# Optimization experiments

Hardware: AMD Instinct MI355X
Metric: run time of the kernel (lower is better)

Reference implementation:

```python
import jax, jax.numpy as jnp
import numpy as np
import math

B, C, H, W = 16, 256, 48, 48
CK = C // 8


def setup_inputs() -> dict:
    key = jax.random.key(0)
    ks = jax.random.split(key, 8)
    s = 0.05
    return {
        "x": jax.random.normal(ks[0], (B, C, H, W), dtype=jnp.float32),
        "Wq": jax.random.normal(ks[1], (CK, C), dtype=jnp.float32) * s,
        "bq": jax.random.normal(ks[2], (CK,), dtype=jnp.float32) * s,
        "Wk": jax.random.normal(ks[3], (CK, C), dtype=jnp.float32) * s,
        "bk": jax.random.normal(ks[4], (CK,), dtype=jnp.float32) * s,
        "Wv": jax.random.normal(ks[5], (C, C), dtype=jnp.float32) * s,
        "bv": jax.random.normal(ks[6], (C,), dtype=jnp.float32) * s,
        "gamma": jax.random.normal(ks[7], (1,), dtype=jnp.float32) * 0.1,
    }


def reference(x, Wq, bq, Wk, bk, Wv, bv, gamma):
    b, c, h, w = x.shape
    n = h * w
    xf = x.reshape(b, c, n)  # [B, C, N] (1x1 conv == channel matmul)
    q = jnp.einsum("oc,bcn->bno", Wq, xf) + bq  # [B, N, C/8]
    k = jnp.einsum("oc,bcn->bon", Wk, xf) + bk[None, :, None]  # [B, C/8, N]
    v = jnp.einsum("oc,bcn->bon", Wv, xf) + bv[None, :, None]  # [B, C, N]
    # NOTE: original scales by sqrt(C) (d_k = C), not sqrt(C//8)
    energy = jnp.einsum("bnd,bdm->bnm", q, k) / math.sqrt(c)  # [B, N, N]
    attn = jax.nn.softmax(energy, axis=-1)
    # out[b,c,i] = sum_j v[b,c,j] * attn[b,i,j]
    out = jnp.einsum("bcj,bij->bci", v, attn).reshape(b, c, h, w)
    return gamma[0] * out + x
```

## Files before the change

### kernel.cpp

```cpp
#include <hip/hip_runtime.h>
#include <hip/hip_bf16.h>

#define Bn  16
#define Cn  256
#define CKn 32
#define Nn  2304

typedef __attribute__((ext_vector_type(16))) float f32x16;
typedef __attribute__((ext_vector_type(8)))  short bf16x8;
typedef __attribute__((ext_vector_type(4)))  int   i32x4;

union FragU { unsigned u[4]; bf16x8 v; };
union KU    { i32x4 i; bf16x8 v; };

__device__ __forceinline__ unsigned pk(float lo, float hi){
  unsigned a = (unsigned)__bfloat16_as_ushort(__float2bfloat16(lo));
  unsigned b = (unsigned)__bfloat16_as_ushort(__float2bfloat16(hi));
  return a | (b << 16);
}

__device__ __forceinline__ void halfswap(unsigned A, unsigned Bv, int ,
                                         unsigned &w0, unsigned &w2){
  asm("v_permlane32_swap_b32 %0, %1" : "+v"(A), "+v"(Bv));
  w0 = A; w2 = Bv;
}

__device__ __forceinline__ void conv_store(const f32x16& a, int h, int l,
                                           __hip_bfloat16* dst0, size_t stride){
  unsigned Wp[8];
  #pragma unroll
  for (int q = 0; q < 8; ++q) Wp[q] = pk(a[2*q], a[2*q+1]);
  #pragma unroll
  for (int k2 = 0; k2 < 2; ++k2){
    FragU u;
    halfswap(Wp[4*k2+0], Wp[4*k2+2], h, u.u[0], u.u[2]);
    halfswap(Wp[4*k2+1], Wp[4*k2+3], h, u.u[1], u.u[3]);
    *(bf16x8*)(dst0 + k2*stride + l*8) = u.v;
  }
}

__device__ __forceinline__ void gld16(const void* g, void* l){
  __builtin_amdgcn_global_load_lds(
      (__attribute__((address_space(1))) void*)const_cast<void*>(g),
      (__attribute__((address_space(3))) void*)l, 16, 0, 0);
}

__global__ __launch_bounds__(64) void wfrag_kernel(
    const float* __restrict__ Wq, const float* __restrict__ bq,
    const float* __restrict__ Wk, const float* __restrict__ bk,
    const float* __restrict__ Wv, const float* __restrict__ bv,
    __hip_bfloat16* __restrict__ Wf){
  const int kt = blockIdx.x / 10, tile = blockIdx.x % 10;
  const int l = threadIdx.x, lo = l & 31, h = l >> 5;
  __hip_bfloat16* dst = Wf + (size_t)(kt*10 + tile)*512 + l*8;
  if (kt < 16){
    const float* Wp; int row;
    if (tile < 8)       { Wp = Wv; row = tile*32 + lo; }
    else if (tile == 8) { Wp = Wq; row = lo; }
    else                { Wp = Wk; row = lo; }
    #pragma unroll
    for (int e = 0; e < 8; ++e)
      dst[e] = __float2bfloat16(Wp[(size_t)row*Cn + kt*16 + 8*h + e]);
  } else {
    const float* bp = tile < 8 ? bv : (tile == 8 ? bq : bk);
    int row = tile < 8 ? tile*32 + lo : lo;
    #pragma unroll
    for (int e = 0; e < 8; ++e)
      dst[e] = __float2bfloat16((h == 0 && e == 0) ? bp[row] : 0.f);
  }
}

__global__ __launch_bounds__(64) void proj_kernel(
    const float* __restrict__ x, const __hip_bfloat16* __restrict__ Wf,
    __hip_bfloat16* __restrict__ Qf, __hip_bfloat16* __restrict__ Kf,
    __hip_bfloat16* __restrict__ Vf){
  const int u = blockIdx.x;
  const int b = u / 72, n32 = u % 72;
  const int l = threadIdx.x & 63, lo = l & 31, h = l >> 5;
  const int n0 = n32*32;

  f32x16 acc[10];
  #pragma unroll
  for (int t = 0; t < 10; ++t)
    #pragma unroll
    for (int r = 0; r < 16; ++r) acc[t][r] = 0.f;

  const float* xb = x + (size_t)b*Cn*Nn + n0 + lo;

  #pragma unroll 1
  for (int kt = 0; kt < 16; ++kt){
    FragU xf;
    float v[8];
    #pragma unroll
    for (int e = 0; e < 8; ++e) v[e] = xb[(size_t)(kt*16 + 8*h + e)*Nn];
    #pragma unroll
    for (int q = 0; q < 4; ++q) xf.u[q] = pk(v[2*q], v[2*q+1]);
    const __hip_bfloat16* wfp = Wf + (size_t)(kt*10)*512 + l*8;
    #pragma unroll
    for (int t = 0; t < 10; ++t){
      bf16x8 wf = *(const bf16x8*)(wfp + t*512);
      if (t < 8) acc[t] = __builtin_amdgcn_mfma_f32_32x32x16_bf16(xf.v, wf, acc[t], 0,0,0);
      else       acc[t] = __builtin_amdgcn_mfma_f32_32x32x16_bf16(wf, xf.v, acc[t], 0,0,0);
    }
  }
  {
    FragU xf;
    xf.u[0] = h ? 0u : 0x00003f80u;
    xf.u[1] = xf.u[2] = xf.u[3] = 0u;
    const __hip_bfloat16* wfp = Wf + (size_t)(16*10)*512 + l*8;
    #pragma unroll
    for (int t = 0; t < 10; ++t){
      bf16x8 wf = *(const bf16x8*)(wfp + t*512);
      if (t < 8) acc[t] = __builtin_amdgcn_mfma_f32_32x32x16_bf16(xf.v, wf, acc[t], 0,0,0);
      else       acc[t] = __builtin_amdgcn_mfma_f32_32x32x16_bf16(wf, xf.v, acc[t], 0,0,0);
    }
  }

  #pragma unroll
  for (int r = 0; r < 16; ++r) acc[8][r] *= 0.09016844f;

  #pragma unroll
  for (int t = 0; t < 8; ++t)
    conv_store(acc[t], h, l, Vf + (((size_t)b*144 + n32*2)*8 + t)*512, 8*512);
  conv_store(acc[8], h, l, Qf + ((size_t)b*72 + n32)*2*512, 512);
  conv_store(acc[9], h, l, Kf + ((size_t)b*72 + n32)*2*512, 512);
}

__global__ __launch_bounds__(128, 2) void attn_kernel(
    const __hip_bfloat16* __restrict__ Qf, const __hip_bfloat16* __restrict__ Kf,
    const __hip_bfloat16* __restrict__ Vf, const float* __restrict__ x,
    const float* __restrict__ gptr, float* __restrict__ out){
  __shared__ __align__(16) char smem[32768];
  const int xcd = blockIdx.x & 7, seq = blockIdx.x >> 3;
  const int b    = xcd*2 + (seq / 72);
  const int rem  = seq % 72;
  const int qb   = rem >> 1;
  const int ch   = rem & 1;
  const int tid = threadIdx.x;
  const int w = tid >> 6, l = tid & 63, lo = l & 31, h = l >> 5;

  const char* vlane = (const char*)Vf + ((size_t)b*1152 + ch*4)*1024 + (size_t)l*16;
  const char* klane = (const char*)Kf + (size_t)b*147456 + (size_t)l*16;

  auto stageV = [&](int jt, int buf){
    const char* gt = vlane + (size_t)jt*32768;
    #pragma unroll
    for (int r = 0; r < 8; ++r){
      const int f = r*2 + w;
      gld16(gt + (f >> 2)*8192 + (f & 3)*1024, smem + buf*16384 + f*1024);
    }
  };
  auto kload = [&](int jn, KU (&kf)[2][2]){
    const char* ka = klane + (size_t)jn*4096;
    asm volatile("global_load_dwordx4 %0, %1, off"             : "=v"(kf[0][0].i) : "v"(ka) : "memory");
    asm volatile("global_load_dwordx4 %0, %1, off offset:1024" : "=v"(kf[0][1].i) : "v"(ka) : "memory");
    asm volatile("global_load_dwordx4 %0, %1, off offset:2048" : "=v"(kf[1][0].i) : "v"(ka) : "memory");
    asm volatile("global_load_dwordx4 %0, %1, off offset:3072" : "=v"(kf[1][1].i) : "v"(ka) : "memory");
  };

  bf16x8 qf[2];
  #pragma unroll
  for (int kt = 0; kt < 2; ++kt)
    qf[kt] = *(const bf16x8*)(Qf + (((size_t)b*72 + qb*2 + w)*2 + kt)*512 + l*8);

  f32x16 acc4[4];
  #pragma unroll
  for (int c = 0; c < 4; ++c)
    #pragma unroll
    for (int r = 0; r < 16; ++r) acc4[c][r] = 0.f;
  float lsum = 0.f;

  KU kfA[2][2], kfB[2][2];

  kload(0, kfA);
  stageV(0, 0);
  kload(1, kfB);

  auto body = [&](int jt, KU (&cur)[2][2], int vb){
    asm volatile("s_waitcnt vmcnt(4)" ::: "memory");
    __builtin_amdgcn_s_barrier();
    __builtin_amdgcn_sched_barrier(0);
    int jn = jt + 1; if (jn >= 36) jn -= 36;
    stageV(jn, vb ^ 1);

    f32x16 z;
    #pragma unroll
    for (int r = 0; r < 16; ++r) z[r] = 0.f;
    f32x16 S0 = __builtin_amdgcn_mfma_f32_32x32x16_bf16(cur[0][0].v, qf[0], z, 0,0,0);
    S0 = __builtin_amdgcn_mfma_f32_32x32x16_bf16(cur[0][1].v, qf[1], S0, 0,0,0);
    f32x16 S1 = __builtin_amdgcn_mfma_f32_32x32x16_bf16(cur[1][0].v, qf[0], z, 0,0,0);
    S1 = __builtin_amdgcn_mfma_f32_32x32x16_bf16(cur[1][1].v, qf[1], S1, 0,0,0);

    int j2 = jt + 2; if (j2 >= 36) j2 -= 36;
    kload(j2, cur);

    FragU pf[4];
    float s0 = 0.f, s1 = 0.f, s2 = 0.f, s3 = 0.f;
    {
      unsigned Wp[8];
      #pragma unroll
      for (int q = 0; q < 4; ++q){
        float p0 = __builtin_amdgcn_exp2f(S0[2*q]);
        float p1 = __builtin_amdgcn_exp2f(S0[2*q+1]);
        s0 += p0 + p1; Wp[q] = pk(p0, p1);
      }
      #pragma unroll
      for (int q = 4; q < 8; ++q){
        float p0 = __builtin_amdgcn_exp2f(S0[2*q]);
        float p1 = __builtin_amdgcn_exp2f(S0[2*q+1]);
        s1 += p0 + p1; Wp[q] = pk(p0, p1);
      }
      halfswap(Wp[0], Wp[2], h, pf[0].u[0], pf[0].u[2]);
      halfswap(Wp[1], Wp[3], h, pf[0].u[1], pf[0].u[3]);
      halfswap(Wp[4], Wp[6], h, pf[1].u[0], pf[1].u[2]);
      halfswap(Wp[5], Wp[7], h, pf[1].u[1], pf[1].u[3]);
    }
    {
      unsigned Wp[8];
      #pragma unroll
      for (int q = 0; q < 4; ++q){
        float p0 = __builtin_amdgcn_exp2f(S1[2*q]);
        float p1 = __builtin_amdgcn_exp2f(S1[2*q+1]);
        s2 += p0 + p1; Wp[q] = pk(p0, p1);
      }
      #pragma unroll
      for (int q = 4; q < 8; ++q){
        float p0 = __builtin_amdgcn_exp2f(S1[2*q]);
        float p1 = __builtin_amdgcn_exp2f(S1[2*q+1]);
        s3 += p0 + p1; Wp[q] = pk(p0, p1);
      }
      halfswap(Wp[0], Wp[2], h, pf[2].u[0], pf[2].u[2]);
      halfswap(Wp[1], Wp[3], h, pf[2].u[1], pf[2].u[3]);
      halfswap(Wp[4], Wp[6], h, pf[3].u[0], pf[3].u[2]);
      halfswap(Wp[5], Wp[7], h, pf[3].u[1], pf[3].u[3]);
    }
    lsum += (s0 + s1) + (s2 + s3);

    const char* cbV = smem + vb*16384;
    #pragma unroll
    for (int js = 0; js < 4; ++js){
      #pragma unroll
      for (int c = 0; c < 4; ++c){
        bf16x8 v = *(const bf16x8*)(cbV + (js*4 + c)*1024 + l*16);
        acc4[c] = __builtin_amdgcn_mfma_f32_32x32x16_bf16(v, pf[js].v, acc4[c], 0,0,0);
      }
    }
  };

  #pragma unroll 1
  for (int jt = 0; jt < 36; jt += 2){
    body(jt,   kfA, 0);
    body(jt+1, kfB, 1);
  }

  lsum += __shfl_xor(lsum, 32);
  const float sc = gptr[0] / lsum;
  const int ibase = qb*64 + w*32;
  #pragma unroll
  for (int c = 0; c < 4; ++c){
    #pragma unroll
    for (int r = 0; r < 16; ++r){
      const int cg = ch*128 + c*32 + (r & 3) + 8*(r >> 2) + 4*h;
      const size_t idx = ((size_t)b*Cn + cg)*Nn + ibase + lo;
      out[idx] = acc4[c][r]*sc + x[idx];
    }
  }
}

extern "C" void kernel_launch(void* const* d_in, const int* in_sizes, int n_in,
                              void* d_out, int out_size, void* d_ws, size_t ws_size,
                              hipStream_t stream) {
  const float* x     = (const float*)d_in[0];
  const float* Wq    = (const float*)d_in[1];
  const float* bq    = (const float*)d_in[2];
  const float* Wk    = (const float*)d_in[3];
  const float* bk    = (const float*)d_in[4];
  const float* Wv    = (const float*)d_in[5];
  const float* bv    = (const float*)d_in[6];
  const float* gamma = (const float*)d_in[7];
  float* out = (float*)d_out;

  __hip_bfloat16* Qf = (__hip_bfloat16*)d_ws;
  __hip_bfloat16* Kf = Qf + (size_t)Bn*72*2*512;
  __hip_bfloat16* Vf = Kf + (size_t)Bn*72*2*512;
  __hip_bfloat16* Wf = Vf + (size_t)Bn*144*8*512;

  wfrag_kernel<<<dim3(170), dim3(64), 0, stream>>>(Wq, bq, Wk, bk, Wv, bv, Wf);
  proj_kernel<<<dim3(1152), dim3(64), 0, stream>>>(x, Wf, Qf, Kf, Vf);
  attn_kernel<<<dim3(1152), dim3(128), 0, stream>>>(Qf, Kf, Vf, x, gamma, out);
}
```

Measured before the change: 107.2 us.

## Split attention blocks to single-wave with unshared single-buffered V staging

The attention kernel moves from 128-thread blocks (two waves sharing a double-buffered 32KB LDS V tile) to 64-thread single-wave blocks, each covering one 32-row query tile, launched as twice as many blocks. Each wave stages its own V tile into a single 16KB buffer and replaces the block barrier with vmcnt/lgkmcnt waits, prefetching K one step ahead instead of two. This removes cross-wave barriers and lets more blocks fit per CU. In exchange, V traffic from L2 per query row doubles, and single buffering exposes V load latency within each iteration.

```diff
diff --git a/kernel.cpp b/kernel.cpp
--- a/kernel.cpp
+++ b/kernel.cpp
@@ -126,29 +126,26 @@
   conv_store(acc[9], h, l, Kf + ((size_t)b*72 + n32)*2*512, 512);
 }
 
-__global__ __launch_bounds__(128, 2) void attn_kernel(
+__global__ __launch_bounds__(64, 2) void attn_kernel(
     const __hip_bfloat16* __restrict__ Qf, const __hip_bfloat16* __restrict__ Kf,
     const __hip_bfloat16* __restrict__ Vf, const float* __restrict__ x,
     const float* __restrict__ gptr, float* __restrict__ out){
-  __shared__ __align__(16) char smem[32768];
+  __shared__ __align__(16) char smem[16384];
   const int xcd = blockIdx.x & 7, seq = blockIdx.x >> 3;
-  const int b    = xcd*2 + (seq / 72);
-  const int rem  = seq % 72;
-  const int qb   = rem >> 1;
-  const int ch   = rem & 1;
-  const int tid = threadIdx.x;
-  const int w = tid >> 6, l = tid & 63, lo = l & 31, h = l >> 5;
+  const int b   = xcd*2 + (seq / 144);
+  const int rem = seq % 144;
+  const int qt  = rem >> 1;
+  const int ch  = rem & 1;
+  const int l = threadIdx.x & 63, lo = l & 31, h = l >> 5;
 
   const char* vlane = (const char*)Vf + ((size_t)b*1152 + ch*4)*1024 + (size_t)l*16;
   const char* klane = (const char*)Kf + (size_t)b*147456 + (size_t)l*16;
 
-  auto stageV = [&](int jt, int buf){
+  auto stageV = [&](int jt){
     const char* gt = vlane + (size_t)jt*32768;
     #pragma unroll
-    for (int r = 0; r < 8; ++r){
-      const int f = r*2 + w;
-      gld16(gt + (f >> 2)*8192 + (f & 3)*1024, smem + buf*16384 + f*1024);
-    }
+    for (int f = 0; f < 16; ++f)
+      gld16(gt + (f >> 2)*8192 + (f & 3)*1024, smem + f*1024);
   };
   auto kload = [&](int jn, KU (&kf)[2][2]){
     const char* ka = klane + (size_t)jn*4096;
@@ -161,7 +158,7 @@
   bf16x8 qf[2];
   #pragma unroll
   for (int kt = 0; kt < 2; ++kt)
-    qf[kt] = *(const bf16x8*)(Qf + (((size_t)b*72 + qb*2 + w)*2 + kt)*512 + l*8);
+    qf[kt] = *(const bf16x8*)(Qf + (((size_t)b*72 + qt)*2 + kt)*512 + l*8);
 
   f32x16 acc4[4];
   #pragma unroll
@@ -171,17 +168,15 @@
   float lsum = 0.f;
 
   KU kfA[2][2], kfB[2][2];
-
   kload(0, kfA);
-  stageV(0, 0);
-  kload(1, kfB);
-
-  auto body = [&](int jt, KU (&cur)[2][2], int vb){
-    asm volatile("s_waitcnt vmcnt(4)" ::: "memory");
-    __builtin_amdgcn_s_barrier();
+
+  auto body = [&](int jt, KU (&cur)[2][2], KU (&nxt)[2][2]){
+    asm volatile("s_waitcnt lgkmcnt(0)" ::: "memory");
+    stageV(jt);
+    int jn = jt + 1; if (jn >= 36) jn = 0;
+    kload(jn, nxt);
+    asm volatile("s_waitcnt vmcnt(20)" ::: "memory");
     __builtin_amdgcn_sched_barrier(0);
-    int jn = jt + 1; if (jn >= 36) jn -= 36;
-    stageV(jn, vb ^ 1);
 
     f32x16 z;
     #pragma unroll
@@ -191,9 +186,6 @@
     f32x16 S1 = __builtin_amdgcn_mfma_f32_32x32x16_bf16(cur[1][0].v, qf[0], z, 0,0,0);
     S1 = __builtin_amdgcn_mfma_f32_32x32x16_bf16(cur[1][1].v, qf[1], S1, 0,0,0);
 
-    int j2 = jt + 2; if (j2 >= 36) j2 -= 36;
-    kload(j2, cur);
-
     FragU pf[4];
     float s0 = 0.f, s1 = 0.f, s2 = 0.f, s3 = 0.f;
     {
@@ -236,12 +228,13 @@
     }
     lsum += (s0 + s1) + (s2 + s3);
 
-    const char* cbV = smem + vb*16384;
+    asm volatile("s_waitcnt vmcnt(4)" ::: "memory");
+    __builtin_amdgcn_sched_barrier(0);
     #pragma unroll
     for (int js = 0; js < 4; ++js){
       #pragma unroll
       for (int c = 0; c < 4; ++c){
-        bf16x8 v = *(const bf16x8*)(cbV + (js*4 + c)*1024 + l*16);
+        bf16x8 v = *(const bf16x8*)(smem + (js*4 + c)*1024 + l*16);
         acc4[c] = __builtin_amdgcn_mfma_f32_32x32x16_bf16(v, pf[js].v, acc4[c], 0,0,0);
       }
     }
@@ -249,13 +242,13 @@
 
   #pragma unroll 1
   for (int jt = 0; jt < 36; jt += 2){
-    body(jt,   kfA, 0);
-    body(jt+1, kfB, 1);
+    body(jt,   kfA, kfB);
+    body(jt+1, kfB, kfA);
   }
 
   lsum += __shfl_xor(lsum, 32);
   const float sc = gptr[0] / lsum;
-  const int ibase = qb*64 + w*32;
+  const int ibase = qt*32;
   #pragma unroll
   for (int c = 0; c < 4; ++c){
     #pragma unroll
@@ -287,5 +280,5 @@
 
   wfrag_kernel<<<dim3(170), dim3(64), 0, stream>>>(Wq, bq, Wk, bk, Wv, bv, Wf);
   proj_kernel<<<dim3(1152), dim3(64), 0, stream>>>(x, Wf, Qf, Kf, Vf);
-  attn_kernel<<<dim3(1152), dim3(128), 0, stream>>>(Qf, Kf, Vf, x, gamma, out);
-}
+  attn_kernel<<<dim3(2304), dim3(64), 0, stream>>>(Qf, Kf, Vf, x, gamma, out);
+}
```

Result: slower. 113.0 us (+5.4%).
